# Performance work log

Measured on AMD Instinct MI355X. Metric: run time of the kernel, lower is better.

## Reference

```python
import jax, jax.numpy as jnp
import numpy as np

NH = 8          # number of attention heads
RAND_P = 0.1    # random attention probability
EPS = 1e-5      # LayerNorm eps (torch default)


def _layer_norm(x, g, b):
    m = x.mean(-1, keepdims=True)
    v = ((x - m) ** 2).mean(-1, keepdims=True)
    return (x - m) * jax.lax.rsqrt(v + EPS) * g + b


def _make_mask(u, n_frames, spatial):
    # random(0/1) + tiled-eye position mask + block-diagonal frame mask (additive float mask)
    L = n_frames * spatial
    idx = jnp.arange(L)
    frame_id = idx // spatial
    pos_id = idx % spatial
    rand = (u >= RAND_P).astype(jnp.float32)
    pos = (pos_id[:, None] == pos_id[None, :]).astype(jnp.float32)
    frame = (frame_id[:, None] == frame_id[None, :]).astype(jnp.float32)
    return rand + pos + frame  # [L, L], values in {0,1,2,3}


def _attn_block(f, u, Wqkv, bqkv, Wo, bo, g1, b1, Wfc1, bfc1, Wfc2, bfc2, g2, b2):
    N, C, H, W = f.shape
    S = H * W
    L = N * S
    hd = C // NH
    src = f.transpose(0, 2, 3, 1).reshape(L, C)  # (n,h,w) flatten order, batch=1 squeezed
    mask = _make_mask(u, N, S)

    qkv = src @ Wqkv.T + bqkv                    # [L, 3C]
    q, k, v = jnp.split(qkv, 3, axis=-1)
    q = q.reshape(L, NH, hd).transpose(1, 0, 2) * (hd ** -0.5)  # [H, L, hd]
    k = k.reshape(L, NH, hd).transpose(1, 0, 2)
    v = v.reshape(L, NH, hd).transpose(1, 0, 2)

    scores = jnp.einsum('hqd,hkd->hqk', q, k) + mask[None]      # [H, L, L]
    attn = jax.nn.softmax(scores, axis=-1)
    o = jnp.einsum('hqk,hkd->hqd', attn, v).transpose(1, 0, 2).reshape(L, C)
    src2 = o @ Wo.T + bo

    x = _layer_norm(src + src2, g1, b1)          # residual + LN (dropout p=0 -> identity)
    h = jax.nn.relu(x @ Wfc1.T + bfc1)
    x = _layer_norm(x + h @ Wfc2.T + bfc2, g2, b2)
    return x.reshape(N, H, W, C).transpose(0, 3, 1, 2)


def setup_inputs() -> dict:
    key = jax.random.key(0)
    ks = jax.random.split(key, 12)
    D = 256
    s = 0.02
    return {
        'f0': jax.random.normal(ks[0], (2, D, 80, 80), jnp.float32),
        'f1': jax.random.normal(ks[1], (2, D, 40, 40), jnp.float32),
        'f2': jax.random.normal(ks[2], (2, D, 32, 32), jnp.float32),
        'f3': jax.random.normal(ks[3], (2, D, 16, 16), jnp.float32),
        'u2': jax.random.uniform(ks[4], (2048, 2048), jnp.float32),
        'u3': jax.random.uniform(ks[5], (512, 512), jnp.float32),
        'Wqkv': jax.random.normal(ks[6], (3 * D, D), jnp.float32) * s,
        'bqkv': jnp.zeros((3 * D,), jnp.float32),
        'Wo': jax.random.normal(ks[7], (D, D), jnp.float32) * s,
        'bo': jnp.zeros((D,), jnp.float32),
        'g1': jnp.ones((D,), jnp.float32),
        'b1': jnp.zeros((D,), jnp.float32),
        'Wfc1': jax.random.normal(ks[8], (4 * D, D), jnp.float32) * s,
        'bfc1': jnp.zeros((4 * D,), jnp.float32),
        'Wfc2': jax.random.normal(ks[9], (D, 4 * D), jnp.float32) * s,
        'bfc2': jnp.zeros((D,), jnp.float32),
        'g2': jnp.ones((D,), jnp.float32),
        'b2': jnp.zeros((D,), jnp.float32),
    }


def reference(f0, f1, f2, f3, u2, u3, Wqkv, bqkv, Wo, bo, g1, b1,
              Wfc1, bfc1, Wfc2, bfc2, g2, b2):
    params = (Wqkv, bqkv, Wo, bo, g1, b1, Wfc1, bfc1, Wfc2, bfc2, g2, b2)
    # levels 0 and 1 pass through untouched (loop starts at i=2)
    out2 = _attn_block(f2, u2, *params)
    out3 = _attn_block(f3, u3, *params)
    return (f0, f1, out2, out3)
```

## Files before the change

### kernel.cpp

```cpp
#include <hip/hip_runtime.h>
#include <hip/hip_bf16.h>
#include <cstddef>


typedef __attribute__((ext_vector_type(8))) short s16x8;
typedef __attribute__((ext_vector_type(4))) short s16x4;
typedef __attribute__((ext_vector_type(4))) float f32x4;
typedef __attribute__((ext_vector_type(2))) unsigned int u32x2;
typedef unsigned short ushort_t;
typedef unsigned long long u64;

#define RTOT 2560

__device__ inline unsigned short f2bf(float x) {
    union { __hip_bfloat16 h; unsigned short u; } cv;
    cv.h = __float2bfloat16(x);
    return cv.u;
}
__device__ inline float bf2f(unsigned short u) {
    union { unsigned int i; float f; } cv;
    cv.i = ((unsigned int)u) << 16;
    return cv.f;
}

__global__ __launch_bounds__(256) void prep(const float* __restrict__ f0,
                                            const float* __restrict__ f1,
                                            float* __restrict__ outp,
                                            const float* __restrict__ wqkv,
                                            const float* __restrict__ wo,
                                            const float* __restrict__ wfc1,
                                            const float* __restrict__ wfc2,
                                            ushort_t* __restrict__ o1,
                                            ushort_t* __restrict__ o2,
                                            ushort_t* __restrict__ o3,
                                            ushort_t* __restrict__ o4,
                                            const float* __restrict__ u2,
                                            const float* __restrict__ u3,
                                            u64* __restrict__ ub,
                                            const float* __restrict__ f2,
                                            const float* __restrict__ f3,
                                            float* __restrict__ srcf,
                                            ushort_t* __restrict__ srcb) {
    int bid = blockIdx.x;
    int t = threadIdx.x;
    if (bid < 4000) {
        int idx = bid * 256 + t;
        f32x4 v = (idx < 819200) ? ((const f32x4*)f0)[idx]
                                 : ((const f32x4*)f1)[idx - 819200];
        ((f32x4*)outp)[idx] = v;
    } else if (bid < 4768) {
        int i = (bid - 4000) * 256 + t;
        const float* src; ushort_t* dst; int li;
        if (i < 49152)       { src = wqkv; dst = o1; li = i; }
        else if (i < 65536)  { src = wo;   dst = o2; li = i - 49152; }
        else if (i < 131072) { src = wfc1; dst = o3; li = i - 65536; }
        else                 { src = wfc2; dst = o4; li = i - 131072; }
        f32x4 v = ((const f32x4*)src)[li];
        s16x4 r;
        r[0] = (short)f2bf(v[0]); r[1] = (short)f2bf(v[1]);
        r[2] = (short)f2bf(v[2]); r[3] = (short)f2bf(v[3]);
        ((s16x4*)dst)[li] = r;
    } else if (bid < 9120) {
        int gw = ((bid - 4768) * 256 + t) >> 6;
        int lane = t & 63;
        const float* p;
        u64* dst;
        if (gw < 16384) {
            int row = gw >> 3, ch = gw & 7;
            p = &u2[(size_t)row * 2048 + ch * 256 + lane * 4];
            dst = &ub[(size_t)gw * 4];
        } else {
            int lw = gw - 16384;
            int row = lw >> 1, ch = lw & 1;
            p = &u3[(size_t)row * 512 + ch * 256 + lane * 4];
            dst = &ub[65536 + (size_t)lw * 4];
        }
        f32x4 v = *(const f32x4*)p;
        u64 b0 = __ballot(v[0] >= 0.1f);
        u64 b1 = __ballot(v[1] >= 0.1f);
        u64 b2 = __ballot(v[2] >= 0.1f);
        u64 b3 = __ballot(v[3] >= 0.1f);
        if (lane < 4) {
            u64 bb = (lane == 0) ? b0 : (lane == 1) ? b1 : (lane == 2) ? b2 : b3;
            dst[lane] = bb;
        }
    } else {
        int idx = (bid - 9120) * 256 + t;
        int r = idx >> 8, c = idx & 255;
        float v;
        if (r < 2048) {
            int n = r >> 10, hw = r & 1023;
            v = f2[(size_t)((n * 256 + c) << 10) + hw];
        } else {
            int rl = r - 2048;
            int n = rl >> 8, hw = rl & 255;
            v = f3[(size_t)((n * 256 + c) << 8) + hw];
        }
        srcf[idx] = v;
        srcb[idx] = f2bf(v);
    }
}

#define ASTR 72

template <int EPI>
__global__ __launch_bounds__(256) void gemm64(const ushort_t* __restrict__ A,
                                              const ushort_t* __restrict__ W,
                                              const float* __restrict__ bias,
                                              ushort_t* __restrict__ outb,
                                              int M, int N, int K) {
    __shared__ __align__(16) ushort_t As[2][64 * ASTR];
    __shared__ __align__(16) ushort_t Ws[2][64 * ASTR];

    const int t = threadIdx.x;
    const int w = t >> 6, l = t & 63;
    const int c = l & 15, g = l >> 4;
    const int mh = w >> 1, nh = w & 1;
    const int m0 = blockIdx.y * 64, n0 = blockIdx.x * 64;
    const int srow = t >> 3;
    const int cg8 = (t & 7) * 8;

    const ushort_t* Aip0 = &A[(size_t)(m0 + srow) * K + cg8];
    const ushort_t* Aip1 = &A[(size_t)(m0 + 32 + srow) * K + cg8];
    const ushort_t* Wip0 = &W[(size_t)(n0 + srow) * K + cg8];
    const ushort_t* Wip1 = &W[(size_t)(n0 + 32 + srow) * K + cg8];

    s16x8 ra0 = *(const s16x8*)Aip0;
    s16x8 ra1 = *(const s16x8*)Aip1;
    s16x8 rw0 = *(const s16x8*)Wip0;
    s16x8 rw1 = *(const s16x8*)Wip1;
    *(s16x8*)&As[0][srow * ASTR + cg8] = ra0;
    *(s16x8*)&As[0][(32 + srow) * ASTR + cg8] = ra1;
    *(s16x8*)&Ws[0][srow * ASTR + cg8] = rw0;
    *(s16x8*)&Ws[0][(32 + srow) * ASTR + cg8] = rw1;
    __syncthreads();

    f32x4 acc[2][2] = {{{0.f,0.f,0.f,0.f},{0.f,0.f,0.f,0.f}},
                       {{0.f,0.f,0.f,0.f},{0.f,0.f,0.f,0.f}}};
    const int nsteps = K >> 6;

    for (int ks = 0; ks < nsteps; ++ks) {
        const int b = ks & 1;
        const bool pf = (ks + 1 < nsteps);
        if (pf) {
            int ko = (ks + 1) << 6;
            ra0 = *(const s16x8*)(Aip0 + ko);
            ra1 = *(const s16x8*)(Aip1 + ko);
            rw0 = *(const s16x8*)(Wip0 + ko);
            rw1 = *(const s16x8*)(Wip1 + ko);
        }
#pragma unroll
        for (int sl = 0; sl < 2; ++sl) {
            s16x8 af0 = *(const s16x8*)&As[b][(32 * mh + c) * ASTR + sl * 32 + 8 * g];
            s16x8 af1 = *(const s16x8*)&As[b][(32 * mh + 16 + c) * ASTR + sl * 32 + 8 * g];
            s16x8 wf0 = *(const s16x8*)&Ws[b][(32 * nh + c) * ASTR + sl * 32 + 8 * g];
            s16x8 wf1 = *(const s16x8*)&Ws[b][(32 * nh + 16 + c) * ASTR + sl * 32 + 8 * g];
            acc[0][0] = __builtin_amdgcn_mfma_f32_16x16x32_bf16(af0, wf0, acc[0][0], 0, 0, 0);
            acc[0][1] = __builtin_amdgcn_mfma_f32_16x16x32_bf16(af0, wf1, acc[0][1], 0, 0, 0);
            acc[1][0] = __builtin_amdgcn_mfma_f32_16x16x32_bf16(af1, wf0, acc[1][0], 0, 0, 0);
            acc[1][1] = __builtin_amdgcn_mfma_f32_16x16x32_bf16(af1, wf1, acc[1][1], 0, 0, 0);
        }
        if (pf) {
            int nb = b ^ 1;
            *(s16x8*)&As[nb][srow * ASTR + cg8] = ra0;
            *(s16x8*)&As[nb][(32 + srow) * ASTR + cg8] = ra1;
            *(s16x8*)&Ws[nb][srow * ASTR + cg8] = rw0;
            *(s16x8*)&Ws[nb][(32 + srow) * ASTR + cg8] = rw1;
        }
        __syncthreads();
    }

#pragma unroll
    for (int i = 0; i < 2; ++i)
#pragma unroll
    for (int j = 0; j < 2; ++j) {
        int n = n0 + 32 * nh + 16 * j + c;
        float bv = bias[n];
        float sc = 1.f;
        if (EPI == 3) sc = (n < 256) ? 0.17677669529663687f : 1.f;
#pragma unroll
        for (int r = 0; r < 4; ++r) {
            int m = m0 + 32 * mh + 16 * i + 4 * g + r;
            float v = acc[i][j][r] + bv;
            if (EPI == 1) v = fmaxf(v, 0.f);
            if (EPI == 3) v *= sc;
            outb[(size_t)m * N + n] = f2bf(v);
        }
    }
}

__global__ __launch_bounds__(128) void gemm_fc2(const ushort_t* __restrict__ A,
                                                const ushort_t* __restrict__ W,
                                                const float* __restrict__ bias,
                                                const float* __restrict__ res,
                                                float* __restrict__ outf,
                                                int M, int N, int K) {
    __shared__ __align__(16) ushort_t As[2][32 * ASTR];
    __shared__ __align__(16) ushort_t Ws[2][32 * ASTR];

    const int t = threadIdx.x;
    const int w = t >> 6, l = t & 63;
    const int c = l & 15, g = l >> 4;
    const int m0 = blockIdx.y * 32, n0 = blockIdx.x * 32;
    const int srow = t >> 3;
    const int cg8 = (t & 7) * 8;

    const ushort_t* Aip0 = &A[(size_t)(m0 + srow) * K + cg8];
    const ushort_t* Aip1 = &A[(size_t)(m0 + 16 + srow) * K + cg8];
    const ushort_t* Wip0 = &W[(size_t)(n0 + srow) * K + cg8];
    const ushort_t* Wip1 = &W[(size_t)(n0 + 16 + srow) * K + cg8];

    s16x8 ra0 = *(const s16x8*)Aip0;
    s16x8 ra1 = *(const s16x8*)Aip1;
    s16x8 rw0 = *(const s16x8*)Wip0;
    s16x8 rw1 = *(const s16x8*)Wip1;
    *(s16x8*)&As[0][srow * ASTR + cg8] = ra0;
    *(s16x8*)&As[0][(16 + srow) * ASTR + cg8] = ra1;
    *(s16x8*)&Ws[0][srow * ASTR + cg8] = rw0;
    *(s16x8*)&Ws[0][(16 + srow) * ASTR + cg8] = rw1;
    __syncthreads();

    f32x4 acc[2] = {{0.f, 0.f, 0.f, 0.f}, {0.f, 0.f, 0.f, 0.f}};
    const int nsteps = K >> 6;

    for (int ks = 0; ks < nsteps; ++ks) {
        const int b = ks & 1;
        const bool pf = (ks + 1 < nsteps);
        if (pf) {
            int ko = (ks + 1) << 6;
            ra0 = *(const s16x8*)(Aip0 + ko);
            ra1 = *(const s16x8*)(Aip1 + ko);
            rw0 = *(const s16x8*)(Wip0 + ko);
            rw1 = *(const s16x8*)(Wip1 + ko);
        }
#pragma unroll
        for (int kt = 0; kt < 2; ++kt) {
            s16x8 af = *(const s16x8*)&As[b][(16 * w + c) * ASTR + kt * 32 + 8 * g];
            s16x8 wf0 = *(const s16x8*)&Ws[b][c * ASTR + kt * 32 + 8 * g];
            s16x8 wf1 = *(const s16x8*)&Ws[b][(16 + c) * ASTR + kt * 32 + 8 * g];
            acc[0] = __builtin_amdgcn_mfma_f32_16x16x32_bf16(af, wf0, acc[0], 0, 0, 0);
            acc[1] = __builtin_amdgcn_mfma_f32_16x16x32_bf16(af, wf1, acc[1], 0, 0, 0);
        }
        if (pf) {
            int nb = b ^ 1;
            *(s16x8*)&As[nb][srow * ASTR + cg8] = ra0;
            *(s16x8*)&As[nb][(16 + srow) * ASTR + cg8] = ra1;
            *(s16x8*)&Ws[nb][srow * ASTR + cg8] = rw0;
            *(s16x8*)&Ws[nb][(16 + srow) * ASTR + cg8] = rw1;
        }
        __syncthreads();
    }

#pragma unroll
    for (int nt = 0; nt < 2; ++nt) {
        int n = n0 + 16 * nt + c;
        float bv = bias[n];
#pragma unroll
        for (int r = 0; r < 4; ++r) {
            int m = m0 + 16 * w + 4 * g + r;
            float v = acc[nt][r] + bv + res[(size_t)m * N + n];
            outf[(size_t)m * N + n] = v;
        }
    }
}

__global__ __launch_bounds__(128) void gemm_wo(const ushort_t* __restrict__ Opart,
                                               const float2* __restrict__ ml,
                                               const ushort_t* __restrict__ W,
                                               const float* __restrict__ bias,
                                               const float* __restrict__ res,
                                               float* __restrict__ outf) {
    const int K = 256, N = 256;
    __shared__ __align__(16) ushort_t As[2][32 * ASTR];
    __shared__ __align__(16) ushort_t Ws[2][32 * ASTR];

    const int t = threadIdx.x;
    const int w = t >> 6, l = t & 63;
    const int c = l & 15, g = l >> 4;
    const int m0 = blockIdx.y * 32, n0 = blockIdx.x * 32;
    const int srow = t >> 3;
    const int cg8 = (t & 7) * 8;

    auto loadA = [&](int row, int kcol) -> s16x8 {
        int head = kcol >> 5;
        float2 a0 = ml[((size_t)0 * RTOT + row) * 8 + head];
        float2 a1 = ml[((size_t)1 * RTOT + row) * 8 + head];
        float2 a2 = ml[((size_t)2 * RTOT + row) * 8 + head];
        float2 a3 = ml[((size_t)3 * RTOT + row) * 8 + head];
        float M = fmaxf(fmaxf(a0.x, a1.x), fmaxf(a2.x, a3.x));
        float w1 = __expf(a0.x - M), w2 = __expf(a1.x - M);
        float w3 = __expf(a2.x - M), w4 = __expf(a3.x - M);
        float inv = 1.f / (w1 * a0.y + w2 * a1.y + w3 * a2.y + w4 * a3.y);
        const size_t str = (size_t)RTOT * 256;
        size_t base = (size_t)row * 256 + kcol;
        s16x8 o1 = *(const s16x8*)&Opart[base];
        s16x8 o2 = *(const s16x8*)&Opart[base + str];
        s16x8 o3 = *(const s16x8*)&Opart[base + 2 * str];
        s16x8 o4 = *(const s16x8*)&Opart[base + 3 * str];
        s16x8 r;
#pragma unroll
        for (int e = 0; e < 8; ++e) {
            float v = w1 * bf2f((ushort_t)o1[e]) + w2 * bf2f((ushort_t)o2[e])
                    + w3 * bf2f((ushort_t)o3[e]) + w4 * bf2f((ushort_t)o4[e]);
            r[e] = (short)f2bf(v * inv);
        }
        return r;
    };

    const ushort_t* Wip0 = &W[(size_t)(n0 + srow) * K + cg8];
    const ushort_t* Wip1 = &W[(size_t)(n0 + 16 + srow) * K + cg8];

    s16x8 ra0 = loadA(m0 + srow, cg8);
    s16x8 ra1 = loadA(m0 + 16 + srow, cg8);
    s16x8 rw0 = *(const s16x8*)Wip0;
    s16x8 rw1 = *(const s16x8*)Wip1;
    *(s16x8*)&As[0][srow * ASTR + cg8] = ra0;
    *(s16x8*)&As[0][(16 + srow) * ASTR + cg8] = ra1;
    *(s16x8*)&Ws[0][srow * ASTR + cg8] = rw0;
    *(s16x8*)&Ws[0][(16 + srow) * ASTR + cg8] = rw1;
    __syncthreads();

    f32x4 acc[2] = {{0.f, 0.f, 0.f, 0.f}, {0.f, 0.f, 0.f, 0.f}};
    const int nsteps = 4;

    for (int ks = 0; ks < nsteps; ++ks) {
        const int b = ks & 1;
        const bool pf = (ks + 1 < nsteps);
        if (pf) {
            int ko = (ks + 1) << 6;
            ra0 = loadA(m0 + srow, ko + cg8);
            ra1 = loadA(m0 + 16 + srow, ko + cg8);
            rw0 = *(const s16x8*)(Wip0 + ko);
            rw1 = *(const s16x8*)(Wip1 + ko);
        }
#pragma unroll
        for (int kt = 0; kt < 2; ++kt) {
            s16x8 af = *(const s16x8*)&As[b][(16 * w + c) * ASTR + kt * 32 + 8 * g];
            s16x8 wf0 = *(const s16x8*)&Ws[b][c * ASTR + kt * 32 + 8 * g];
            s16x8 wf1 = *(const s16x8*)&Ws[b][(16 + c) * ASTR + kt * 32 + 8 * g];
            acc[0] = __builtin_amdgcn_mfma_f32_16x16x32_bf16(af, wf0, acc[0], 0, 0, 0);
            acc[1] = __builtin_amdgcn_mfma_f32_16x16x32_bf16(af, wf1, acc[1], 0, 0, 0);
        }
        if (pf) {
            int nb = b ^ 1;
            *(s16x8*)&As[nb][srow * ASTR + cg8] = ra0;
            *(s16x8*)&As[nb][(16 + srow) * ASTR + cg8] = ra1;
            *(s16x8*)&Ws[nb][srow * ASTR + cg8] = rw0;
            *(s16x8*)&Ws[nb][(16 + srow) * ASTR + cg8] = rw1;
        }
        __syncthreads();
    }

#pragma unroll
    for (int nt = 0; nt < 2; ++nt) {
        int n = n0 + 16 * nt + c;
        float bv = bias[n];
#pragma unroll
        for (int r = 0; r < 4; ++r) {
            int m = m0 + 16 * w + 4 * g + r;
            outf[(size_t)m * 256 + n] = acc[nt][r] + bv + res[(size_t)m * 256 + n];
        }
    }
}

#define KS 40
#define VS 66
#define PS 72
#define OS 68

__global__ __launch_bounds__(256) void flash_split(const ushort_t* __restrict__ qkvb,
                                                   const u64* __restrict__ ubits,
                                                   ushort_t* __restrict__ Opart,
                                                   float2* __restrict__ ml) {
    __shared__ __align__(16) ushort_t ks[2][64 * KS];
    __shared__ __align__(16) ushort_t vts[2][32 * VS];
    __shared__ __align__(16) char pso[64 * PS * 2];
    ushort_t* ps = (ushort_t*)pso;
    float* os = (float*)pso;

    const int bx = blockIdx.x;
    int qt, h, split, L, sshift, rowbase;
    const u64* ub;
    if (bx < 1024) {
        qt = bx & 31; h = (bx >> 5) & 7; split = bx >> 8;
        L = 2048; sshift = 10; rowbase = 0; ub = ubits;
    } else {
        int lo = bx - 1024;
        qt = lo & 7; h = (lo >> 3) & 7; split = lo >> 6;
        L = 512; sshift = 8; rowbase = 2048; ub = ubits + 65536;
    }
    const int tps = (L >> 6) >> 2;
    const int ts0 = split * tps;
    const int nch = L >> 8;

    const int t = threadIdx.x;
    const int w = t >> 6;
    const int l = t & 63;
    const int c = l & 15;
    const int g = l >> 4;
    const int smask = (1 << sshift) - 1;

    const int srow = t >> 2;
    const int sc8 = (t & 3) * 8;
    const int q0g = rowbase + qt * 64;

    const int ql = qt * 64 + 16 * w + c;
    const s16x8 qf = *(const s16x8*)&qkvb[(size_t)(rowbase + ql) * 768 + h * 32 + 8 * g];
    const int qp = ql & smask, qfr = ql >> sshift;
    const u64* ubq = &ub[(size_t)ql * nch * 4];

    s16x8 kreg, vreg;
    {
        size_t base = (size_t)(rowbase + ts0 * 64 + srow) * 768 + h * 32 + sc8;
        s16x8 k0r = *(const s16x8*)&qkvb[base + 256];
        s16x8 v0r = *(const s16x8*)&qkvb[base + 512];
        *(s16x8*)&ks[0][srow * KS + sc8] = k0r;
#pragma unroll
        for (int i = 0; i < 8; ++i)
            vts[0][(sc8 + i) * VS + srow] = (ushort_t)v0r[i];
        if (tps > 1) {
            kreg = *(const s16x8*)&qkvb[base + 64 * 768 + 256];
            vreg = *(const s16x8*)&qkvb[base + 64 * 768 + 512];
        }
    }
    __syncthreads();

    f32x4 oacc0 = {0.f, 0.f, 0.f, 0.f};
    f32x4 oacc1 = {0.f, 0.f, 0.f, 0.f};
    float mold = -3e38f, lrun = 0.f;
    const f32x4 zc = {0.f, 0.f, 0.f, 0.f};

    u64 wr0 = 0, wr1 = 0, wr2 = 0, wr3 = 0;
    int cur = 0;
    for (int kt = 0; kt < tps; ++kt) {
        const int nxt = cur ^ 1;
        const int gt = ts0 + kt;
        const int k0 = gt << 6;

        if (kt + 1 < tps) {
            *(s16x8*)&ks[nxt][srow * KS + sc8] = kreg;
#pragma unroll
            for (int i = 0; i < 8; ++i)
                vts[nxt][(sc8 + i) * VS + srow] = (ushort_t)vreg[i];
        }
        if (kt + 2 < tps) {
            size_t base = (size_t)(rowbase + (gt + 2) * 64 + srow) * 768 + h * 32 + sc8;
            kreg = *(const s16x8*)&qkvb[base + 256];
            vreg = *(const s16x8*)&qkvb[base + 512];
        }

        if ((gt & 3) == 0 || kt == 0) {
            const u64* bp = &ubq[(size_t)(gt >> 2) * 4];
            wr0 = bp[0]; wr1 = bp[1]; wr2 = bp[2]; wr3 = bp[3];
        }
        const unsigned shb = 16 * (gt & 3);

        f32x4 sacc[4];
#pragma unroll
        for (int nt = 0; nt < 4; ++nt) {
            s16x8 kf = *(const s16x8*)&ks[cur][(16 * nt + c) * KS + 8 * g];
            sacc[nt] = __builtin_amdgcn_mfma_f32_16x16x32_bf16(kf, qf, zc, 0, 0, 0);
        }

        float sv[4][4];
        float m = -3e38f;
#pragma unroll
        for (int nt = 0; nt < 4; ++nt) {
            unsigned sh = shb + 4 * nt + g;
#pragma unroll
            for (int r = 0; r < 4; ++r) {
                u64 wrd = (r == 0) ? wr0 : (r == 1) ? wr1 : (r == 2) ? wr2 : wr3;
                int kg = k0 + 16 * nt + 4 * g + r;
                float s = sacc[nt][r]
                        + ((wrd >> sh) & 1 ? 1.f : 0.f)
                        + ((kg & smask) == qp ? 1.f : 0.f)
                        + ((kg >> sshift) == qfr ? 1.f : 0.f);
                sv[nt][r] = s;
                m = fmaxf(m, s);
            }
        }
        m = fmaxf(m, __shfl_xor(m, 16));
        m = fmaxf(m, __shfl_xor(m, 32));
        float newm = fmaxf(mold, m);
        float fac = __expf(mold - newm);
        mold = newm;

        float sum = 0.f;
#pragma unroll
        for (int nt = 0; nt < 4; ++nt) {
            float p0 = __expf(sv[nt][0] - newm);
            float p1 = __expf(sv[nt][1] - newm);
            float p2 = __expf(sv[nt][2] - newm);
            float p3 = __expf(sv[nt][3] - newm);
            sum += (p0 + p1) + (p2 + p3);
            u32x2 pk;
            pk[0] = ((unsigned)f2bf(p1) << 16) | f2bf(p0);
            pk[1] = ((unsigned)f2bf(p3) << 16) | f2bf(p2);
            *(u32x2*)&ps[(16 * w + c) * PS + 16 * nt + 4 * g] = pk;
        }
        sum += __shfl_xor(sum, 16);
        sum += __shfl_xor(sum, 32);
        lrun = lrun * fac + sum;
        oacc0 *= fac;
        oacc1 *= fac;

#pragma unroll
        for (int kc = 0; kc < 2; ++kc) {
            s16x8 pfr = *(const s16x8*)&ps[(16 * w + c) * PS + 32 * kc + 8 * g];
            s16x8 vf0 = *(const s16x8*)&vts[cur][c * VS + 32 * kc + 8 * g];
            s16x8 vf1 = *(const s16x8*)&vts[cur][(16 + c) * VS + 32 * kc + 8 * g];
            oacc0 = __builtin_amdgcn_mfma_f32_16x16x32_bf16(vf0, pfr, oacc0, 0, 0, 0);
            oacc1 = __builtin_amdgcn_mfma_f32_16x16x32_bf16(vf1, pfr, oacc1, 0, 0, 0);
        }

        __syncthreads();
        cur = nxt;
    }

    if (g == 0) {
        int q = q0g + 16 * w + c;
        ml[((size_t)split * RTOT + q) * 8 + h] = make_float2(mold, lrun);
    }

#pragma unroll
    for (int r = 0; r < 4; ++r) {
        os[(4 * g + r) * OS + 16 * w + c] = oacc0[r];
        os[(16 + 4 * g + r) * OS + 16 * w + c] = oacc1[r];
    }
    __syncthreads();
    {
        int r = t >> 2, d0 = (t & 3) * 8;
        s16x8 pk;
#pragma unroll
        for (int i = 0; i < 8; ++i) pk[i] = (short)f2bf(os[(d0 + i) * OS + r]);
        *(s16x8*)&Opart[((size_t)split * RTOT + q0g + r) * 256 + h * 32 + d0] = pk;
    }
}

__global__ __launch_bounds__(256) void ln1_kernel(const float* __restrict__ in,
                                                  const float* __restrict__ g,
                                                  const float* __restrict__ b,
                                                  float* __restrict__ outf,
                                                  ushort_t* __restrict__ outb) {
    __shared__ float red[256];
    int row = blockIdx.x, t = threadIdx.x;
    float v = in[(size_t)row * 256 + t];
    red[t] = v;
    __syncthreads();
    for (int s = 128; s > 0; s >>= 1) {
        if (t < s) red[t] += red[t + s];
        __syncthreads();
    }
    float mean = red[0] * (1.f / 256.f);
    __syncthreads();
    float d = v - mean;
    red[t] = d * d;
    __syncthreads();
    for (int s = 128; s > 0; s >>= 1) {
        if (t < s) red[t] += red[t + s];
        __syncthreads();
    }
    float var = red[0] * (1.f / 256.f);
    float r = d * rsqrtf(var + 1e-5f) * g[t] + b[t];
    outf[(size_t)row * 256 + t] = r;
    outb[(size_t)row * 256 + t] = f2bf(r);
}

__global__ __launch_bounds__(256) void ln2_out(const float* __restrict__ in,
                                               const float* __restrict__ g,
                                               const float* __restrict__ b,
                                               float* __restrict__ out2,
                                               float* __restrict__ out3) {
    __shared__ float red[256];
    int row = blockIdx.x, t = threadIdx.x;
    float v = in[(size_t)row * 256 + t];
    red[t] = v;
    __syncthreads();
    for (int s = 128; s > 0; s >>= 1) {
        if (t < s) red[t] += red[t + s];
        __syncthreads();
    }
    float mean = red[0] * (1.f / 256.f);
    __syncthreads();
    float d = v - mean;
    red[t] = d * d;
    __syncthreads();
    for (int s = 128; s > 0; s >>= 1) {
        if (t < s) red[t] += red[t + s];
        __syncthreads();
    }
    float var = red[0] * (1.f / 256.f);
    float r = d * rsqrtf(var + 1e-5f) * g[t] + b[t];
    if (row < 2048) {
        int n = row >> 10, hw = row & 1023;
        out2[((size_t)(n * 256 + t) << 10) + hw] = r;
    } else {
        int rl = row - 2048;
        int n = rl >> 8, hw = rl & 255;
        out3[((size_t)(n * 256 + t) << 8) + hw] = r;
    }
}


extern "C" void kernel_launch(void* const* d_in, const int* in_sizes, int n_in,
                              void* d_out, int out_size, void* d_ws, size_t ws_size,
                              hipStream_t stream) {
    const float* f0 = (const float*)d_in[0];
    const float* f1 = (const float*)d_in[1];
    const float* f2 = (const float*)d_in[2];
    const float* f3 = (const float*)d_in[3];
    const float* u2 = (const float*)d_in[4];
    const float* u3 = (const float*)d_in[5];
    const float* Wqkv = (const float*)d_in[6];
    const float* bqkv = (const float*)d_in[7];
    const float* Wo   = (const float*)d_in[8];
    const float* bo   = (const float*)d_in[9];
    const float* g1   = (const float*)d_in[10];
    const float* b1   = (const float*)d_in[11];
    const float* Wfc1 = (const float*)d_in[12];
    const float* bfc1 = (const float*)d_in[13];
    const float* Wfc2 = (const float*)d_in[14];
    const float* bfc2 = (const float*)d_in[15];
    const float* g2   = (const float*)d_in[16];
    const float* b2   = (const float*)d_in[17];

    float* out = (float*)d_out;
    float* ws = (float*)d_ws;

    ushort_t* wqkv = (ushort_t*)ws;
    ushort_t* wo   = (ushort_t*)(ws + 98304);
    ushort_t* wfc1 = (ushort_t*)(ws + 131072);
    ushort_t* wfc2 = (ushort_t*)(ws + 262144);

    float* sc = ws + 393216;
    float*    src_f32 = sc;
    ushort_t* qkvb    = (ushort_t*)(sc + 655360);
    ushort_t* src_bf  = (ushort_t*)(sc + 1638400);
    float*    t1      = sc + 1966080;
    float*    x_f32   = sc + 2621440;
    u64*      ubits   = (u64*)x_f32;
    ushort_t* x_bf    = (ushort_t*)(sc + 3276800);
    float2*   ml      = (float2*)(sc + 3604480);
    ushort_t* Opart   = (ushort_t*)(sc + 3768320);
    ushort_t* h_bf    = Opart;

    prep<<<11680, 256, 0, stream>>>(f0, f1, out,
                                    Wqkv, Wo, Wfc1, Wfc2, wqkv, wo, wfc1, wfc2,
                                    u2, u3, ubits, f2, f3, src_f32, src_bf);

    gemm64<3><<<dim3(12, 40), 256, 0, stream>>>(
        src_bf, wqkv, bqkv, qkvb, RTOT, 768, 256);
    flash_split<<<1280, 256, 0, stream>>>(qkvb, ubits, Opart, ml);
    gemm_wo<<<dim3(8, 80), 128, 0, stream>>>(Opart, ml, wo, bo, src_f32, t1);
    ln1_kernel<<<2560, 256, 0, stream>>>(t1, g1, b1, x_f32, x_bf);
    gemm64<1><<<dim3(16, 40), 256, 0, stream>>>(
        x_bf, wfc1, bfc1, h_bf, RTOT, 1024, 256);
    gemm_fc2<<<dim3(8, 80), 128, 0, stream>>>(
        h_bf, wfc2, bfc2, x_f32, t1, RTOT, 256, 1024);
    ln2_out<<<2560, 256, 0, stream>>>(t1, g2, b2, out + 4096000, out + 4620288);
}
```

Before: 93.90 us.

## Double flash split-K to 8 partitions and tile-transpose the NCHW input in prep

Raises the flash-attention key split from 4 to 8 partitions, doubling the block count so more CUs stay busy, and generalises the merge in the Wo GEMM prologue to combine 8 partial outputs. It also rewrites the NCHW-to-row-major source transpose in prep to go through a padded 64x64 shared-memory tile, so both reads and writes are coalesced. In exchange, the Wo prologue reads twice as much partial-output data and ml/Opart scratch grows, which is why Opart is moved.

```diff
diff --git a/kernel.cpp b/kernel.cpp
--- a/kernel.cpp
+++ b/kernel.cpp
@@ -11,6 +11,7 @@
 typedef unsigned long long u64;
 
 #define RTOT 2560
+#define NSPLIT 8
 
 __device__ inline unsigned short f2bf(float x) {
     union { __hip_bfloat16 h; unsigned short u; } cv;
@@ -41,6 +42,7 @@
                                             const float* __restrict__ f3,
                                             float* __restrict__ srcf,
                                             ushort_t* __restrict__ srcb) {
+    __shared__ float tl[64][65];
     int bid = blockIdx.x;
     int t = threadIdx.x;
     if (bid < 4000) {
@@ -85,19 +87,32 @@
             dst[lane] = bb;
         }
     } else {
-        int idx = (bid - 9120) * 256 + t;
-        int r = idx >> 8, c = idx & 255;
-        float v;
-        if (r < 2048) {
-            int n = r >> 10, hw = r & 1023;
-            v = f2[(size_t)((n * 256 + c) << 10) + hw];
+        int b = bid - 9120;
+        const float* src; int S, rowb, n, ct, ht;
+        if (b < 128) {
+            n = b >> 6; int rem = b & 63; ct = rem >> 4; ht = rem & 15;
+            src = f2; S = 1024; rowb = 0;
         } else {
-            int rl = r - 2048;
-            int n = rl >> 8, hw = rl & 255;
-            v = f3[(size_t)((n * 256 + c) << 8) + hw];
-        }
-        srcf[idx] = v;
-        srcb[idx] = f2bf(v);
+            int b2 = b - 128;
+            n = b2 >> 4; int rem = b2 & 15; ct = rem >> 2; ht = rem & 3;
+            src = f3; S = 256; rowb = 2048;
+        }
+        int c0 = ct * 64, hw0 = ht * 64;
+        int i = t >> 6, lane = t & 63;
+#pragma unroll
+        for (int jj = 0; jj < 16; ++jj) {
+            int cl = i * 16 + jj;
+            tl[lane][cl] = src[(size_t)(n * 256 + c0 + cl) * S + hw0 + lane];
+        }
+        __syncthreads();
+#pragma unroll
+        for (int jj = 0; jj < 16; ++jj) {
+            int hl = i * 16 + jj;
+            int row = rowb + n * S + hw0 + hl;
+            float v = tl[hl][lane];
+            srcf[(size_t)row * 256 + c0 + lane] = v;
+            srcb[(size_t)row * 256 + c0 + lane] = f2bf(v);
+        }
     }
 }
 
@@ -283,27 +298,33 @@
 
     auto loadA = [&](int row, int kcol) -> s16x8 {
         int head = kcol >> 5;
-        float2 a0 = ml[((size_t)0 * RTOT + row) * 8 + head];
-        float2 a1 = ml[((size_t)1 * RTOT + row) * 8 + head];
-        float2 a2 = ml[((size_t)2 * RTOT + row) * 8 + head];
-        float2 a3 = ml[((size_t)3 * RTOT + row) * 8 + head];
-        float M = fmaxf(fmaxf(a0.x, a1.x), fmaxf(a2.x, a3.x));
-        float w1 = __expf(a0.x - M), w2 = __expf(a1.x - M);
-        float w3 = __expf(a2.x - M), w4 = __expf(a3.x - M);
-        float inv = 1.f / (w1 * a0.y + w2 * a1.y + w3 * a2.y + w4 * a3.y);
+        float2 a[NSPLIT];
+        float M = -3e38f;
+#pragma unroll
+        for (int s = 0; s < NSPLIT; ++s) {
+            a[s] = ml[((size_t)s * RTOT + row) * 8 + head];
+            M = fmaxf(M, a[s].x);
+        }
+        float wgt[NSPLIT];
+        float denom = 0.f;
+#pragma unroll
+        for (int s = 0; s < NSPLIT; ++s) {
+            wgt[s] = __expf(a[s].x - M);
+            denom += wgt[s] * a[s].y;
+        }
+        float inv = 1.f / denom;
         const size_t str = (size_t)RTOT * 256;
         size_t base = (size_t)row * 256 + kcol;
-        s16x8 o1 = *(const s16x8*)&Opart[base];
-        s16x8 o2 = *(const s16x8*)&Opart[base + str];
-        s16x8 o3 = *(const s16x8*)&Opart[base + 2 * str];
-        s16x8 o4 = *(const s16x8*)&Opart[base + 3 * str];
+        float acc[8] = {};
+#pragma unroll
+        for (int s = 0; s < NSPLIT; ++s) {
+            s16x8 o = *(const s16x8*)&Opart[base + s * str];
+#pragma unroll
+            for (int e = 0; e < 8; ++e) acc[e] += wgt[s] * bf2f((ushort_t)o[e]);
+        }
         s16x8 r;
 #pragma unroll
-        for (int e = 0; e < 8; ++e) {
-            float v = w1 * bf2f((ushort_t)o1[e]) + w2 * bf2f((ushort_t)o2[e])
-                    + w3 * bf2f((ushort_t)o3[e]) + w4 * bf2f((ushort_t)o4[e]);
-            r[e] = (short)f2bf(v * inv);
-        }
+        for (int e = 0; e < 8; ++e) r[e] = (short)f2bf(acc[e] * inv);
         return r;
     };
 
@@ -381,15 +402,15 @@
     const int bx = blockIdx.x;
     int qt, h, split, L, sshift, rowbase;
     const u64* ub;
-    if (bx < 1024) {
+    if (bx < 2048) {
         qt = bx & 31; h = (bx >> 5) & 7; split = bx >> 8;
         L = 2048; sshift = 10; rowbase = 0; ub = ubits;
     } else {
-        int lo = bx - 1024;
+        int lo = bx - 2048;
         qt = lo & 7; h = (lo >> 3) & 7; split = lo >> 6;
         L = 512; sshift = 8; rowbase = 2048; ub = ubits + 65536;
     }
-    const int tps = (L >> 6) >> 2;
+    const int tps = (L >> 6) >> 3;
     const int ts0 = split * tps;
     const int nch = L >> 8;
 
@@ -641,16 +662,16 @@
     u64*      ubits   = (u64*)x_f32;
     ushort_t* x_bf    = (ushort_t*)(sc + 3276800);
     float2*   ml      = (float2*)(sc + 3604480);
-    ushort_t* Opart   = (ushort_t*)(sc + 3768320);
+    ushort_t* Opart   = (ushort_t*)(sc + 3932160);
     ushort_t* h_bf    = Opart;
 
-    prep<<<11680, 256, 0, stream>>>(f0, f1, out,
-                                    Wqkv, Wo, Wfc1, Wfc2, wqkv, wo, wfc1, wfc2,
-                                    u2, u3, ubits, f2, f3, src_f32, src_bf);
+    prep<<<9280, 256, 0, stream>>>(f0, f1, out,
+                                   Wqkv, Wo, Wfc1, Wfc2, wqkv, wo, wfc1, wfc2,
+                                   u2, u3, ubits, f2, f3, src_f32, src_bf);
 
     gemm64<3><<<dim3(12, 40), 256, 0, stream>>>(
         src_bf, wqkv, bqkv, qkvb, RTOT, 768, 256);
-    flash_split<<<1280, 256, 0, stream>>>(qkvb, ubits, Opart, ml);
+    flash_split<<<2560, 256, 0, stream>>>(qkvb, ubits, Opart, ml);
     gemm_wo<<<dim3(8, 80), 128, 0, stream>>>(Opart, ml, wo, bo, src_f32, t1);
     ln1_kernel<<<2560, 256, 0, stream>>>(t1, g1, b1, x_f32, x_bf);
     gemm64<1><<<dim3(16, 40), 256, 0, stream>>>(
```

Result: slower. 101.6 us (+8.2%).
